# Optimization experiments

Measured on AMD Instinct MI355X. Metric: run time of the kernel, lower is better.

## Reference

```python
import math
import jax, jax.numpy as jnp
import numpy as np

B, N, DIM = 2, 4096, 768
H, DK, DV = 8, 64, 64


def setup_inputs() -> dict:
    key = jax.random.key(0)
    ks = jax.random.split(key, 6)
    s = 0.02
    return {
        "x": jax.random.normal(ks[0], (B, N, DIM), dtype=jnp.float32),
        "Wq": jax.random.normal(ks[1], (DIM, H * DK), dtype=jnp.float32) * s,
        "Wk": jax.random.normal(ks[2], (DIM, H * DK), dtype=jnp.float32) * s,
        "Wv": jax.random.normal(ks[3], (DIM, H * DV), dtype=jnp.float32) * s,
        "Wo": jax.random.normal(ks[4], (H * DV, DIM), dtype=jnp.float32) * s,
        "bo": jax.random.normal(ks[5], (DIM,), dtype=jnp.float32) * s,
    }


def reference(x, Wq, Wk, Wv, Wo, bo):
    b, n, _ = x.shape
    # project and split heads: [B, H, N, d]
    q = (x @ Wq).reshape(b, n, H, DK).transpose(0, 2, 1, 3)
    k = (x @ Wk).reshape(b, n, H, DK).transpose(0, 2, 1, 3)
    v = (x @ Wv).reshape(b, n, H, DV).transpose(0, 2, 1, 3)
    scale = 1.0 / math.sqrt(DK)
    scores = jnp.einsum("bhnd,bhmd->bhnm", q, k) * scale  # [B,H,N,N]
    attn = jax.nn.softmax(scores, axis=-1)
    out = jnp.einsum("bhnm,bhmd->bhnd", attn, v)  # [B,H,N,DV]
    out = out.transpose(0, 2, 1, 3).reshape(b, n, H * DV)
    return out @ Wo + bo
```

## Files before the change

### kernel.cpp

```cpp
#include <hip/hip_runtime.h>
#include <hip/hip_bf16.h>

#define B_   2
#define N_   4096
#define DIM_ 768
#define H_   8
#define MROWS_ 8192

typedef __bf16 bf16x8 __attribute__((ext_vector_type(8)));
typedef __bf16 bf16x4 __attribute__((ext_vector_type(4)));
typedef float  f32x4  __attribute__((ext_vector_type(4)));

static __device__ __forceinline__ f32x4 mfma16(bf16x8 a, bf16x8 b, f32x4 c) {
    return __builtin_amdgcn_mfma_f32_16x16x32_bf16(a, b, c, 0, 0, 0);
}

#define GLDS16(g, l) \
    __builtin_amdgcn_global_load_lds((const __attribute__((address_space(1))) void*)(g), \
                                     (__attribute__((address_space(3))) void*)(l), 16, 0, 0)

__global__ void cvt_x_kernel(const float* __restrict__ x, __bf16* __restrict__ xb, int n4) {
    int i = blockIdx.x * blockDim.x + threadIdx.x;
    if (i >= n4) return;
    float4 f = reinterpret_cast<const float4*>(x)[i];
    bf16x4 o;
    o[0] = (__bf16)f.x; o[1] = (__bf16)f.y; o[2] = (__bf16)f.z; o[3] = (__bf16)f.w;
    reinterpret_cast<bf16x4*>(xb)[i] = o;
}

__global__ __launch_bounds__(256) void transpose_w_kernel(const float* __restrict__ Wq,
                                                          const float* __restrict__ Wk,
                                                          const float* __restrict__ Wv,
                                                          const float* __restrict__ Wo,
                                                          __bf16* __restrict__ wt,
                                                          __bf16* __restrict__ wot) {
    __shared__ float tile[64][65];
    const int bix = blockIdx.x;
    const float* src;
    int src_ld, rbase, cbase, dst_ld, drow, dcol;
    __bf16* dst;
    if (bix < 288) {
        int m = bix / 96, t = bix - m * 96;
        int tr = t >> 3, tc = t & 7;
        src = (m == 0) ? Wq : ((m == 1) ? Wk : Wv);
        src_ld = 512; rbase = tr * 64; cbase = tc * 64;
        dst = wt; dst_ld = 768; drow = m * 512 + tc * 64; dcol = tr * 64;
    } else {
        int t = bix - 288;
        int tr = t / 12, tc = t - tr * 12;
        src = Wo; src_ld = 768; rbase = tr * 64; cbase = tc * 64;
        dst = wot; dst_ld = 512; drow = tc * 64; dcol = tr * 64;
    }
#pragma unroll
    for (int kk = 0; kk < 4; ++kk) {
        int idx = threadIdx.x + kk * 256;
        int r = idx >> 4, c = (idx & 15) << 2;
        float4 f = *reinterpret_cast<const float4*>(&src[(size_t)(rbase + r) * src_ld + cbase + c]);
        tile[r][c] = f.x; tile[r][c + 1] = f.y; tile[r][c + 2] = f.z; tile[r][c + 3] = f.w;
    }
    __syncthreads();
#pragma unroll
    for (int kk = 0; kk < 4; ++kk) {
        int idx = threadIdx.x + kk * 256;
        int r = idx >> 4, c = (idx & 15) << 2;
        bf16x4 ov;
        ov[0] = (__bf16)tile[c][r];     ov[1] = (__bf16)tile[c + 1][r];
        ov[2] = (__bf16)tile[c + 2][r]; ov[3] = (__bf16)tile[c + 3][r];
        *reinterpret_cast<bf16x4*>(&dst[(size_t)(drow + r) * dst_ld + dcol + c]) = ov;
    }
}

template<int KSTEPS>
__device__ __forceinline__ void gemm_tile_main(const __bf16* __restrict__ A, const int lda,
                                               const int arow0,
                                               const __bf16* __restrict__ Bt, const int ldb,
                                               const int bcol0,
                                               __bf16* __restrict__ abuf,
                                               __bf16* __restrict__ bbuf,
                                               f32x4 (&acc)[4][4]) {
    const int lane = threadIdx.x & 63, wave = threadIdx.x >> 6;
    const int lr = lane & 15, lg = lane >> 4;
    const int wr = wave >> 1, wc = wave & 1;

    const int cid0 = wave * 128 + lane;
    const int cid1 = cid0 + 64;
    const __bf16* sA0 = A  + (size_t)(arow0 + (cid0 >> 2)) * lda + (cid0 & 3) * 8;
    const __bf16* sA1 = A  + (size_t)(arow0 + (cid1 >> 2)) * lda + (cid1 & 3) * 8;
    const __bf16* sB0 = Bt + (size_t)(bcol0 + (cid0 >> 2)) * ldb + (cid0 & 3) * 8;
    const __bf16* sB1 = Bt + (size_t)(bcol0 + (cid1 >> 2)) * ldb + (cid1 & 3) * 8;

    auto stage = [&](int buf, int ks) {
        __bf16* da = abuf + buf * 4096 + wave * 1024;
        __bf16* db = bbuf + buf * 4096 + wave * 1024;
        GLDS16(sA0 + ks * 32, da);
        GLDS16(sA1 + ks * 32, da + 512);
        GLDS16(sB0 + ks * 32, db);
        GLDS16(sB1 + ks * 32, db + 512);
    };

    stage(0, 0);
    asm volatile("s_waitcnt vmcnt(0)" ::: "memory");
    __syncthreads();

    const int ar_off = (wr * 64 + lr) * 32 + lg * 8;
    const int br_off = (wc * 64 + lr) * 32 + lg * 8;

    int buf = 0;
    for (int ks = 0; ks < KSTEPS; ++ks) {
        if (ks + 1 < KSTEPS) stage(buf ^ 1, ks + 1);
        const __bf16* ab = abuf + buf * 4096 + ar_off;
        const __bf16* bb = bbuf + buf * 4096 + br_off;
        bf16x8 af[4], bfr[4];
#pragma unroll
        for (int m = 0; m < 4; ++m) af[m] = *reinterpret_cast<const bf16x8*>(ab + m * 512);
#pragma unroll
        for (int n = 0; n < 4; ++n) bfr[n] = *reinterpret_cast<const bf16x8*>(bb + n * 512);
#pragma unroll
        for (int m = 0; m < 4; ++m)
#pragma unroll
            for (int n = 0; n < 4; ++n)
                acc[m][n] = mfma16(af[m], bfr[n], acc[m][n]);
        asm volatile("s_waitcnt vmcnt(0)" ::: "memory");
        __syncthreads();
        buf ^= 1;
    }
}

__global__ __launch_bounds__(256) void qkv_gemm_kernel(const __bf16* __restrict__ xb,
                                                       const __bf16* __restrict__ wt,
                                                       __bf16* __restrict__ q,
                                                       __bf16* __restrict__ k,
                                                       __bf16* __restrict__ vt) {
    __shared__ __align__(16) __bf16 abuf[2 * 4096];
    __shared__ __align__(16) __bf16 bbuf[2 * 4096];

    const int bid = blockIdx.x;
    const int vb = (bid & 7) * 96 + (bid >> 3);
    const int by = vb % 12, bx = vb / 12;

    f32x4 acc[4][4] = {};
    gemm_tile_main<24>(xb, 768, bx * 128, wt, 768, by * 128, abuf, bbuf, acc);

    const int lane = threadIdx.x & 63, wave = threadIdx.x >> 6;
    const int lr = lane & 15, lg = lane >> 4;
    const int wr = wave >> 1, wc = wave & 1;
    const int bi = (bx * 128) >> 12;
    const int nbase = (bx * 128) & 4095;

    const float QSCALE = 0.125f * 1.44269504089f;

#pragma unroll
    for (int n = 0; n < 4; ++n) {
        const int col0 = by * 128 + wc * 64 + n * 16;
        const int mtx = col0 >> 9;
        const int h   = (col0 >> 6) & 7;
        const int d0  = (col0 & 63) + lr;
        const size_t hb = (size_t)(bi * 8 + h);
#pragma unroll
        for (int m = 0; m < 4; ++m) {
            const int nn = nbase + wr * 64 + m * 16 + lg * 4;
            if (mtx == 0) {
#pragma unroll
                for (int r = 0; r < 4; ++r)
                    q[(hb * 4096 + nn + r) * 64 + d0] = (__bf16)(acc[m][n][r] * QSCALE);
            } else if (mtx == 1) {
#pragma unroll
                for (int r = 0; r < 4; ++r)
                    k[(hb * 4096 + nn + r) * 64 + d0] = (__bf16)acc[m][n][r];
            } else {
                bf16x4 ov;
#pragma unroll
                for (int r = 0; r < 4; ++r) ov[r] = (__bf16)acc[m][n][r];
                *reinterpret_cast<bf16x4*>(&vt[(hb * 64 + d0) * 4096 + nn]) = ov;
            }
        }
    }
}

__global__ __launch_bounds__(512, 4) void attn_kernel(const __bf16* __restrict__ q,
                                                      const __bf16* __restrict__ k,
                                                      const __bf16* __restrict__ vt,
                                                      __bf16* __restrict__ o) {
    const int lane = threadIdx.x & 63, wave = threadIdx.x >> 6;
    const int lr = lane & 15, lg = lane >> 4;
    const int qg = wave >> 1, kh = wave & 1;

    const int bid  = blockIdx.x;
    const int vbid = (bid & 7) * 64 + (bid >> 3);
    const int qtile = vbid & 31;
    const int bh    = vbid >> 5;
    const int qbase = qtile * 128 + qg * 32;

    const __bf16* Qh = q  + (size_t)bh * N_ * 64;
    const __bf16* Kh = k  + (size_t)bh * N_ * 64;
    const __bf16* Vh = vt + (size_t)bh * 64 * N_;

    __shared__ __align__(16) char smem[32768];
    __bf16* kb0 = (__bf16*)smem;
    __bf16* vb0 = (__bf16*)(smem + 16384);

    const int l8 = lane >> 3, l7 = lane & 7;
    const int swz8 = (l7 ^ l8) * 8;

    int ksrc[2];
#pragma unroll
    for (int c = 0; c < 2; ++c) {
        int i = wave * 16 + c * 8 + l8;
        int sig = ((i >> 4) & 1) * 32 + ((i >> 2) & 3) * 8 + ((i >> 5) & 1) * 4 + (i & 3);
        ksrc[c] = sig * 64 + swz8;
    }

    auto stageK = [&](int buf, int jt) {
        if (wave < 4) {
            const __bf16* srcb = Kh + (size_t)jt * 4096;
            __bf16* dst = kb0 + buf * 4096 + wave * 1024;
            GLDS16(srcb + ksrc[0], dst);
            GLDS16(srcb + ksrc[1], dst + 512);
        }
    };
    auto stageV = [&](int buf, int jt) {
        if (wave >= 4) {
            const int w2 = wave - 4;
            const __bf16* src = Vh + (size_t)(w2 * 16 + l8) * 4096 + jt * 64 + swz8;
            __bf16* dst = vb0 + buf * 4096 + w2 * 1024;
            GLDS16(src, dst);
            GLDS16(src + (size_t)8 * 4096, dst + 512);
        }
    };

    bf16x8 qf[2][2];
#pragma unroll
    for (int f = 0; f < 2; ++f)
#pragma unroll
        for (int kc = 0; kc < 2; ++kc)
            qf[f][kc] = *reinterpret_cast<const bf16x8*>(
                Qh + (size_t)(qbase + f * 16 + lr) * 64 + kc * 32 + lg * 8);

    f32x4 acc[2][4] = {};
    f32x4 accl[2] = {};
    bf16x8 vones;
#pragma unroll
    for (int t = 0; t < 8; ++t) vones[t] = (__bf16)1.0f;

    f32x4 s[2][2];
    bf16x8 pk[2];

    auto QK = [&](const __bf16* kb_) {
        const char* kb = (const char*)kb_;
        __builtin_amdgcn_s_setprio(1);
#pragma unroll
        for (int kc = 0; kc < 2; ++kc) {
#pragma unroll
            for (int c2 = 0; c2 < 2; ++c2) {
                const int row = (kh + 2 * c2) * 16 + lr;
                bf16x8 bk = *reinterpret_cast<const bf16x8*>(
                    kb + row * 128 + (((kc * 4 + lg) ^ (lr & 7)) << 4));
#pragma unroll
                for (int f = 0; f < 2; ++f) {
                    if (kc == 0) s[f][c2] = mfma16(bk, qf[f][0], {});
                    else         s[f][c2] = mfma16(bk, qf[f][1], s[f][c2]);
                }
            }
        }
        __builtin_amdgcn_s_setprio(0);
    };
    auto EXP = [&]() {
#pragma unroll
        for (int f = 0; f < 2; ++f) {
#pragma unroll
            for (int t = 0; t < 8; ++t)
                pk[f][t] = (__bf16)__builtin_amdgcn_exp2f(s[f][t >> 2][t & 3]);
            accl[f] = mfma16(pk[f], vones, accl[f]);
        }
    };
    auto PV = [&](const __bf16* vb_) {
        const char* vb = (const char*)vb_;
        __builtin_amdgcn_s_setprio(1);
#pragma unroll
        for (int cbv = 0; cbv < 4; ++cbv) {
            const int row = cbv * 16 + lr;
            bf16x8 bv = *reinterpret_cast<const bf16x8*>(
                vb + row * 128 + (((kh * 4 + lg) ^ (lr & 7)) << 4));
#pragma unroll
            for (int f = 0; f < 2; ++f)
                acc[f][cbv] = mfma16(pk[f], bv, acc[f][cbv]);
        }
        __builtin_amdgcn_s_setprio(0);
    };

    stageK(0, 0);
    asm volatile("s_waitcnt vmcnt(0)" ::: "memory");
    __syncthreads();

    stageK(1, 1);
    stageV(0, 0);
    QK(kb0);
    EXP();
    asm volatile("s_waitcnt vmcnt(0)" ::: "memory");
    __syncthreads();

    for (int jt = 1; jt < 63; ++jt) {
        stageK((jt + 1) & 1, jt + 1);
        stageV(jt & 1, jt);
        QK(kb0 + (jt & 1) * 4096);
        PV(vb0 + ((jt - 1) & 1) * 4096);
        EXP();
        asm volatile("s_waitcnt vmcnt(0)" ::: "memory");
        __syncthreads();
    }

    stageV(1, 63);
    QK(kb0 + 4096);
    PV(vb0);
    EXP();
    asm volatile("s_waitcnt vmcnt(0)" ::: "memory");
    __syncthreads();

    PV(vb0 + 4096);
    __syncthreads();

    char* exa = smem + qg * 4096;
    char* exl = smem + 16384 + qg * 2048;
    if (kh == 1) {
#pragma unroll
        for (int f = 0; f < 2; ++f) {
#pragma unroll
            for (int cbv = 0; cbv < 4; ++cbv) {
                bf16x4 p4;
#pragma unroll
                for (int r = 0; r < 4; ++r) p4[r] = (__bf16)acc[f][cbv][r];
                *reinterpret_cast<bf16x4*>(exa + lane * 64 + (f * 4 + cbv) * 8) = p4;
            }
            *reinterpret_cast<f32x4*>(exl + lane * 32 + f * 16) = accl[f];
        }
    }
    __syncthreads();

    if (kh == 0) {
        const int b = bh >> 3, h = bh & 7;
#pragma unroll
        for (int f = 0; f < 2; ++f) {
            f32x4 lp = *reinterpret_cast<const f32x4*>(exl + lane * 32 + f * 16);
            f32x4 inv;
#pragma unroll
            for (int r = 0; r < 4; ++r) inv[r] = 1.f / (accl[f][r] + lp[r]);
#pragma unroll
            for (int cbv = 0; cbv < 4; ++cbv) {
                bf16x4 ap = *reinterpret_cast<const bf16x4*>(exa + lane * 64 + (f * 4 + cbv) * 8);
#pragma unroll
                for (int r = 0; r < 4; ++r) {
                    const int row = b * N_ + qbase + f * 16 + lg * 4 + r;
                    o[(size_t)row * 512 + h * 64 + cbv * 16 + lr] =
                        (__bf16)((acc[f][cbv][r] + (float)ap[r]) * inv[r]);
                }
            }
        }
    }
}

__global__ __launch_bounds__(256) void out_gemm_kernel(const __bf16* __restrict__ ob,
                                                       const __bf16* __restrict__ wot,
                                                       const float* __restrict__ bo,
                                                       float* __restrict__ out) {
    __shared__ __align__(16) __bf16 abuf[2 * 4096];
    __shared__ __align__(16) __bf16 bbuf[2 * 4096];

    const int bid = blockIdx.x;
    const int vb = (bid & 7) * 48 + (bid >> 3);
    const int by = vb % 6, bx = vb / 6;

    f32x4 acc[4][4] = {};
    gemm_tile_main<16>(ob, 512, bx * 128, wot, 512, by * 128, abuf, bbuf, acc);

    const int lane = threadIdx.x & 63, wave = threadIdx.x >> 6;
    const int lr = lane & 15, lg = lane >> 4;
    const int wr = wave >> 1, wc = wave & 1;

#pragma unroll
    for (int n = 0; n < 4; ++n) {
        const int col = by * 128 + wc * 64 + n * 16 + lr;
        const float bias = bo[col];
#pragma unroll
        for (int m = 0; m < 4; ++m) {
            const int row0 = bx * 128 + wr * 64 + m * 16 + lg * 4;
#pragma unroll
            for (int r = 0; r < 4; ++r)
                out[(size_t)(row0 + r) * 768 + col] = acc[m][n][r] + bias;
        }
    }
}

extern "C" void kernel_launch(void* const* d_in, const int* in_sizes, int n_in,
                              void* d_out, int out_size, void* d_ws, size_t ws_size,
                              hipStream_t stream) {
    const float* x  = (const float*)d_in[0];
    const float* Wq = (const float*)d_in[1];
    const float* Wk = (const float*)d_in[2];
    const float* Wv = (const float*)d_in[3];
    const float* Wo = (const float*)d_in[4];
    const float* bo = (const float*)d_in[5];
    float* out = (float*)d_out;

    char* ws = (char*)d_ws;
    __bf16* xb  = (__bf16*)(ws);
    __bf16* wt  = (__bf16*)(ws + 12582912);
    __bf16* wot = (__bf16*)(ws + 12582912 + 2359296);
    char*   p0  = ws + 12582912 + 2359296 + 786432;
    __bf16* qw  = (__bf16*)(p0);
    __bf16* kw  = (__bf16*)(p0 + 8388608);
    __bf16* vtw = (__bf16*)(p0 + 2 * (size_t)8388608);
    __bf16* obf = (__bf16*)(p0 + 3 * (size_t)8388608);

    cvt_x_kernel<<<6144, 256, 0, stream>>>(x, xb, MROWS_ * DIM_ / 4);
    transpose_w_kernel<<<384, 256, 0, stream>>>(Wq, Wk, Wv, Wo, wt, wot);
    qkv_gemm_kernel<<<768, 256, 0, stream>>>(xb, wt, qw, kw, vtw);
    attn_kernel<<<512, 512, 0, stream>>>(qw, kw, vtw, obf);
    out_gemm_kernel<<<384, 256, 0, stream>>>(obf, wot, bo, out);
}
```

Measured before the change: 125.5 us.

## Triple-buffer K/V tiles in attention with partial vmcnt waits

Moves the attention K/V LDS staging from double to triple buffering, prefetching two tiles ahead. The per-iteration full vmcnt(0) wait is relaxed to vmcnt(2), and __syncthreads is replaced by a raw s_barrier, so global-to-LDS loads for the next tile stay in flight across the barrier. LDS use rises from 32KB to 48KB per block, which may cut occupancy under launch_bounds(512,4). It also risks races if the vmcnt accounting or the slot rotation is wrong.

```diff
diff --git a/kernel.cpp b/kernel.cpp
--- a/kernel.cpp
+++ b/kernel.cpp
@@ -195,9 +195,9 @@
     const __bf16* Kh = k  + (size_t)bh * N_ * 64;
     const __bf16* Vh = vt + (size_t)bh * 64 * N_;
 
-    __shared__ __align__(16) char smem[32768];
+    __shared__ __align__(16) char smem[49152];
     __bf16* kb0 = (__bf16*)smem;
-    __bf16* vb0 = (__bf16*)(smem + 16384);
+    __bf16* vb0 = (__bf16*)(smem + 24576);
 
     const int l8 = lane >> 3, l7 = lane & 7;
     const int swz8 = (l7 ^ l8) * 8;
@@ -210,19 +210,22 @@
         ksrc[c] = sig * 64 + swz8;
     }
 
-    auto stageK = [&](int buf, int jt) {
+    auto kslot = [&](int s) { return kb0 + s * 4096; };
+    auto vslot = [&](int s) { return vb0 + s * 4096; };
+
+    auto stageK = [&](int slot, int jt) {
         if (wave < 4) {
             const __bf16* srcb = Kh + (size_t)jt * 4096;
-            __bf16* dst = kb0 + buf * 4096 + wave * 1024;
+            __bf16* dst = kslot(slot) + wave * 1024;
             GLDS16(srcb + ksrc[0], dst);
             GLDS16(srcb + ksrc[1], dst + 512);
         }
     };
-    auto stageV = [&](int buf, int jt) {
+    auto stageV = [&](int slot, int jt) {
         if (wave >= 4) {
             const int w2 = wave - 4;
             const __bf16* src = Vh + (size_t)(w2 * 16 + l8) * 4096 + jt * 64 + swz8;
-            __bf16* dst = vb0 + buf * 4096 + w2 * 1024;
+            __bf16* dst = vslot(slot) + w2 * 1024;
             GLDS16(src, dst);
             GLDS16(src + (size_t)8 * 4096, dst + 512);
         }
@@ -288,35 +291,48 @@
         __builtin_amdgcn_s_setprio(0);
     };
 
-    stageK(0, 0);
+    auto ITER = [&](int kr, int kw, int ktile, int vr, int vw, int vtile) {
+        stageK(kw, ktile);
+        stageV(vw, vtile);
+        QK(kslot(kr));
+        PV(vslot(vr));
+        EXP();
+        asm volatile("s_waitcnt vmcnt(2)" ::: "memory");
+        __builtin_amdgcn_s_barrier();
+    };
+
+    stageK(0, 0); stageK(1, 1); stageV(0, 0);
     asm volatile("s_waitcnt vmcnt(0)" ::: "memory");
-    __syncthreads();
-
-    stageK(1, 1);
-    stageV(0, 0);
-    QK(kb0);
+    __builtin_amdgcn_s_barrier();
+
+    stageK(2, 2); stageV(1, 1);
+    QK(kslot(0));
+    EXP();
+    asm volatile("s_waitcnt vmcnt(2)" ::: "memory");
+    __builtin_amdgcn_s_barrier();
+
+    for (int t = 0; t < 20; ++t) {
+        const int a = 3 * t + 1;
+        ITER(1, 0, a + 2, 0, 2, a + 1);
+        ITER(2, 1, a + 3, 1, 0, a + 2);
+        ITER(0, 2, a + 4, 2, 1, a + 3);
+    }
+    ITER(1, 0, 63, 0, 2, 62);
+
+    stageV(0, 63);
+    QK(kslot(2));
+    PV(vslot(1));
     EXP();
     asm volatile("s_waitcnt vmcnt(0)" ::: "memory");
-    __syncthreads();
-
-    for (int jt = 1; jt < 63; ++jt) {
-        stageK((jt + 1) & 1, jt + 1);
-        stageV(jt & 1, jt);
-        QK(kb0 + (jt & 1) * 4096);
-        PV(vb0 + ((jt - 1) & 1) * 4096);
-        EXP();
-        asm volatile("s_waitcnt vmcnt(0)" ::: "memory");
-        __syncthreads();
-    }
-
-    stageV(1, 63);
-    QK(kb0 + 4096);
-    PV(vb0);
+    __builtin_amdgcn_s_barrier();
+
+    QK(kslot(0));
+    PV(vslot(2));
     EXP();
     asm volatile("s_waitcnt vmcnt(0)" ::: "memory");
-    __syncthreads();
-
-    PV(vb0 + 4096);
+    __builtin_amdgcn_s_barrier();
+
+    PV(vslot(0));
     __syncthreads();
 
     char* exa = smem + qg * 4096;
```

New measurement: 122.9 us. 2.1% less time.
